# Kernel tuning notes

Hardware: AMD Instinct MI355X
Metric: run time of the kernel (lower is better)

Reference implementation:

```python
import jax, jax.numpy as jnp
import numpy as np

B, S, D, H, HD = 2, 2048, 1024, 16, 64
K, L = 1024, 4  # num_codes, vq_levels


def setup_inputs() -> dict:
    key = jax.random.key(0)
    ks = jax.random.split(key, 12)
    w = lambda k, shape: jax.random.normal(k, shape, jnp.float32) * 0.02
    return {
        "x": jax.random.normal(ks[0], (B, S, D), jnp.float32),
        "ln1_g": jnp.ones((D,), jnp.float32), "ln1_b": jnp.zeros((D,), jnp.float32),
        "wq": w(ks[1], (D, D)), "wk": w(ks[2], (D, D)), "wv": w(ks[3], (D, D)),
        "wg": w(ks[4], (D, D)), "wo": w(ks[5], (D, D)),
        "ln2_g": jnp.ones((D,), jnp.float32), "ln2_b": jnp.zeros((D,), jnp.float32),
        "w1": w(ks[6], (D, 4 * D)), "b1": jnp.zeros((4 * D,), jnp.float32),
        "w2": w(ks[7], (4 * D, D)), "b2": jnp.zeros((D,), jnp.float32),
        "ln3_g": jnp.ones((D,), jnp.float32), "ln3_b": jnp.zeros((D,), jnp.float32),
        "codebooks": jax.random.uniform(ks[8], (L, K, D), jnp.float32, -1.0 / K, 1.0 / K),
    }


def _ln(x, g, b):
    m = jnp.mean(x, -1, keepdims=True)
    v = jnp.var(x, -1, keepdims=True)
    return (x - m) / jnp.sqrt(v + 1e-5) * g + b


def _rope(x):  # x: [B, S, H, HD]
    hd = x.shape[-1]
    inv = 1.0 / (10000.0 ** (jnp.arange(0, hd, 2, dtype=jnp.float32) / hd))
    t = jnp.arange(x.shape[1], dtype=jnp.float32)
    f = jnp.einsum('i,j->ij', t, inv)               # [S, HD/2]
    emb = jnp.concatenate([f, f], -1)               # [S, HD]
    cos = jnp.cos(emb)[None, :, None, :]
    sin = jnp.sin(emb)[None, :, None, :]
    x1, x2 = jnp.split(x, 2, -1)
    rot = jnp.concatenate([-x2, x1], -1)
    return x * cos + rot * sin


def reference(x, ln1_g, ln1_b, wq, wk, wv, wg, wo, ln2_g, ln2_b,
              w1, b1, w2, b2, ln3_g, ln3_b, codebooks):
    # --- retention sub-block (pre-LN) ---
    h = _ln(x, ln1_g, ln1_b)
    q = (h @ wq).reshape(B, S, H, HD)
    k = (h @ wk).reshape(B, S, H, HD)
    v = (h @ wv).reshape(B, S, H, HD)
    q, k = _rope(q), _rope(k)
    q, k, v = (a.transpose(0, 2, 1, 3) for a in (q, k, v))  # [B,H,S,HD]
    i = jnp.arange(S)
    dmask = jnp.tril(i[:, None] - i[None, :]).astype(jnp.float32)  # [S,S], >=0
    gamma = (1.0 - jnp.exp2(-5.0 - jnp.arange(H, dtype=jnp.float32)))[:, None, None]
    decay = (gamma ** dmask) * jnp.tril(jnp.ones((S, S), jnp.float32))  # [H,S,S]
    ret = jnp.einsum('bhqd,bhkd->bhqk', q, k) / np.sqrt(HD).astype(np.float32) * decay
    o = jnp.einsum('bhqk,bhkd->bhqd', ret, v).transpose(0, 2, 1, 3).reshape(B, S, D)
    g = jax.nn.silu(h @ wg)
    x = x + (o * g) @ wo
    # --- MLP sub-block (pre-LN) ---
    h2 = _ln(x, ln2_g, ln2_b)
    x = x + (jax.nn.gelu(h2 @ w1 + b1, approximate=False) @ w2 + b2)
    # --- residual vector quantizer ---
    xn = _ln(x, ln3_g, ln3_b)
    residual, total = xn, jnp.zeros_like(xn)
    ql, el = 0.0, 0.0
    for lvl in range(L):
        cb = codebooks[lvl]                         # [K, D]
        flat = residual.reshape(-1, D)              # [B*S, D]
        d2 = (jnp.sum(flat ** 2, 1, keepdims=True)
              + jnp.sum(cb ** 2, 1) - 2.0 * flat @ cb.T)
        idx = jnp.argmin(d2, 1)
        quant = cb[idx].reshape(xn.shape)
        ql = ql + jnp.mean((quant - jax.lax.stop_gradient(residual)) ** 2)
        el = el + jnp.mean((jax.lax.stop_gradient(quant) - residual) ** 2)
        total = total + quant
        residual = residual - jax.lax.stop_gradient(quant)
    final = xn + jax.lax.stop_gradient(total - xn)  # straight-through
    return (x + final, ql / L, el / L)
```

## Files before the change

### kernel.cpp

```cpp
#include <hip/hip_runtime.h>
#include <cstdint>
#include <cstddef>

#define DEV __device__ __forceinline__

typedef __attribute__((ext_vector_type(8))) short bf16x8;
typedef __attribute__((ext_vector_type(4))) float f32x4;

typedef const __attribute__((address_space(1))) void gl_void;
typedef __attribute__((address_space(3))) void lds_void;

DEV unsigned short f2bf(float f){
  union { float f; uint32_t u; } v; v.f = f;
  uint32_t r = v.u + 0x7FFFu + ((v.u >> 16) & 1u);
  return (unsigned short)(r >> 16);
}
DEV float bf2f(unsigned short u){
  union { uint32_t u; float f; } v; v.u = ((uint32_t)u) << 16; return v.f;
}
DEV uint32_t packbf2(float a, float b){
  return (uint32_t)f2bf(a) | ((uint32_t)f2bf(b) << 16);
}

__global__ void ln_kernel(const float* __restrict__ x, const float* __restrict__ gw,
                          const float* __restrict__ bw, unsigned short* __restrict__ obf,
                          float* __restrict__ of32)
{
  const int row = blockIdx.x, t = threadIdx.x;
  const float4 v = ((const float4*)(x + (size_t)row*1024))[t];
  float s  = v.x + v.y + v.z + v.w;
  float s2 = v.x*v.x + v.y*v.y + v.z*v.z + v.w*v.w;
  #pragma unroll
  for (int o = 32; o >= 1; o >>= 1){ s += __shfl_down(s, o); s2 += __shfl_down(s2, o); }
  __shared__ float red[8];
  const int w = t >> 6, ln = t & 63;
  if (ln == 0){ red[w] = s; red[4+w] = s2; }
  __syncthreads();
  const float fs  = red[0]+red[1]+red[2]+red[3];
  const float fs2 = red[4]+red[5]+red[6]+red[7];
  const float mean = fs * (1.0f/1024.0f);
  const float var  = fs2 * (1.0f/1024.0f) - mean*mean;
  const float rstd = rsqrtf(var + 1e-5f);
  const float4 gv = ((const float4*)gw)[t];
  const float4 bv = ((const float4*)bw)[t];
  float4 o4;
  o4.x = (v.x-mean)*rstd*gv.x + bv.x;
  o4.y = (v.y-mean)*rstd*gv.y + bv.y;
  o4.z = (v.z-mean)*rstd*gv.z + bv.z;
  o4.w = (v.w-mean)*rstd*gv.w + bv.w;
  if (of32) ((float4*)(of32 + (size_t)row*1024))[t] = o4;
  ushort4 ob; ob.x = f2bf(o4.x); ob.y = f2bf(o4.y); ob.z = f2bf(o4.z); ob.w = f2bf(o4.w);
  ((ushort4*)(obf + (size_t)row*1024))[t] = ob;
}

struct Ptr5 { const float* p[5]; };

DEV void dev_transpose(const float* __restrict__ src, unsigned short* __restrict__ dst,
                       int r0, int c0, int R, int C)
{
  __shared__ float tile[32][33];
  const int tx = threadIdx.x & 31, ty = threadIdx.x >> 5;
  #pragma unroll
  for (int i = 0; i < 32; i += 8)
    tile[ty+i][tx] = src[(size_t)(r0+ty+i)*C + c0 + tx];
  __syncthreads();
  #pragma unroll
  for (int i = 0; i < 32; i += 8)
    dst[(size_t)(c0+ty+i)*R + r0 + tx] = f2bf(tile[tx][ty+i]);
}

__global__ void prep_all(Ptr5 p5, unsigned short* __restrict__ wqkvgT,
                         const float* __restrict__ w1, unsigned short* __restrict__ w1T,
                         const float* __restrict__ w2, unsigned short* __restrict__ w2T,
                         const float* __restrict__ cb, unsigned short* __restrict__ cbbf,
                         float* __restrict__ cbn2, float2* __restrict__ rtab)
{
  const int b = blockIdx.x, t = threadIdx.x;
  if (b < 5120){
    const int z = b >> 10, r = b & 1023;
    dev_transpose(p5.p[z], wqkvgT + (size_t)z*1048576, (r >> 5)*32, (r & 31)*32, 1024, 1024);
  } else if (b < 9216){
    const int r = b - 5120;
    dev_transpose(w1, w1T, (r >> 7)*32, (r & 127)*32, 1024, 4096);
  } else if (b < 13312){
    const int r = b - 9216;
    dev_transpose(w2, w2T, (r >> 5)*32, (r & 31)*32, 4096, 1024);
  } else if (b < 17408){
    const int code = b - 13312;
    const float4 v = ((const float4*)(cb + (size_t)code*1024))[t];
    ushort4 o; o.x = f2bf(v.x); o.y = f2bf(v.y); o.z = f2bf(v.z); o.w = f2bf(v.w);
    ((ushort4*)(cbbf + (size_t)code*1024))[t] = o;
    float s = v.x*v.x + v.y*v.y + v.z*v.z + v.w*v.w;
    #pragma unroll
    for (int off = 32; off >= 1; off >>= 1) s += __shfl_down(s, off);
    __shared__ float red[4];
    if ((t & 63) == 0) red[t >> 6] = s;
    __syncthreads();
    if (t == 0) cbn2[code] = red[0]+red[1]+red[2]+red[3];
  } else {
    const int i = (b - 17408)*256 + t;
    const int s = i >> 5, j = i & 31;
    const float ang = (float)s * exp2f(-(float)j * 0.4152410118609203f);
    float sn, cs; sincosf(ang, &sn, &cs);
    rtab[i] = make_float2(cs, sn);
  }
}

template<int EPI>
__global__ __launch_bounds__(512, 2) void gemm256(
    const unsigned short* __restrict__ A, const unsigned short* __restrict__ BT,
    unsigned short* __restrict__ C, const float* __restrict__ bias,
    const float2* __restrict__ rt, int M, int N, int K)
{
  __shared__ __align__(16) unsigned short SH[65536];
  const int t = threadIdx.x;
  const int w = t >> 6, ln = t & 63, lg = ln >> 4, lc = ln & 15;
  const int wm = w >> 2, wn = w & 3;
  const int gx = gridDim.x, nwg = gridDim.x * gridDim.y;
  int lin = blockIdx.y * gx + blockIdx.x;
  lin = (lin >> 3) + (lin & 7) * (nwg >> 3);
  const int m0 = (lin / gx) * 256, n0 = (lin % gx) * 256;
  const int NT = K >> 6;
  const int nit = NT >> 1;

  f32x4 acc[2][2][4][2] = {};
  bf16x8 aF[4][2], bF[2][2];

  auto stageHT = [&](int d, int isB, int h, int kt){
    const unsigned short* src = isB ? BT : A;
    const int mb = (isB ? n0 : m0) + h*128;
    const int base16 = isB*4096 + d*2048 + h*1024;
    #pragma unroll
    for (int j = 0; j < 2; ++j){
      const int o = j*512 + t;
      const int wu = o & 63;
      const int r16 = wu >> 2, cu = wu & 3;
      const int s = o >> 6;
      const int rg = s >> 1, cg = s & 1;
      const int row = rg*16 + r16;
      const int srcu = cg*4 + (cu ^ ((r16 & 8) >> 2));
      __builtin_amdgcn_global_load_lds(
        (gl_void*)(src + (size_t)(mb + row)*K + (size_t)kt*64 + srcu*8),
        (lds_void*)&SH[(base16 + j*512 + (t & ~63))*8], 16, 0, 0);
    }
  };

  auto ldA = [&](int d, int mh, int mf, int ks) -> bf16x8 {
    const int u = d*2048 + mh*1024 + ((wm*4+mf)*2 + ks)*64 + lc*4 + (lg ^ ((lc & 8) >> 2));
    return *(const bf16x8*)&SH[u*8];
  };
  auto ldB = [&](int d, int nh, int nf, int ks) -> bf16x8 {
    const int u = 4096 + d*2048 + nh*1024 + ((wn*2+nf)*2 + ks)*64 + lc*4 + (lg ^ ((lc & 8) >> 2));
    return *(const bf16x8*)&SH[u*8];
  };

#define RD_A(d, mh) { _Pragma("unroll") for (int mf = 0; mf < 4; ++mf){ \
    aF[mf][0] = ldA(d, mh, mf, 0); aF[mf][1] = ldA(d, mh, mf, 1); } }
#define RD_B(d, nh) { _Pragma("unroll") for (int nf = 0; nf < 2; ++nf){ \
    bF[nf][0] = ldB(d, nh, nf, 0); bF[nf][1] = ldB(d, nh, nf, 1); } }
#define MM(mh, nh) { \
    __builtin_amdgcn_s_setprio(1); \
    _Pragma("unroll") for (int mf = 0; mf < 4; ++mf) \
      _Pragma("unroll") for (int nf = 0; nf < 2; ++nf){ \
        acc[mh][nh][mf][nf] = __builtin_amdgcn_mfma_f32_16x16x32_bf16(aF[mf][0], bF[nf][0], acc[mh][nh][mf][nf], 0, 0, 0); \
        acc[mh][nh][mf][nf] = __builtin_amdgcn_mfma_f32_16x16x32_bf16(aF[mf][1], bF[nf][1], acc[mh][nh][mf][nf], 0, 0, 0); } \
    __builtin_amdgcn_s_setprio(0); }
#define BAR()   __builtin_amdgcn_s_barrier()
#define LGKM0() asm volatile("s_waitcnt lgkmcnt(0)" ::: "memory")

  stageHT(0,0,0,0); stageHT(0,0,1,0); stageHT(0,1,0,0); stageHT(0,1,1,0);
  stageHT(1,0,0,1); stageHT(1,1,1,1);
  asm volatile("s_waitcnt vmcnt(4)" ::: "memory");
  BAR();

  for (int it = 0; it < nit; ++it){
    const int v = 2*it + 1, up = 2*it + 2, vp = 2*it + 3;
    const bool hu = (up < NT), hv = (vp < NT);

    RD_A(0,0); RD_B(0,0);
    stageHT(1,0,1,v);
    BAR(); LGKM0(); MM(0,0); BAR();

    RD_B(0,1);
    stageHT(1,1,0,v);
    BAR(); LGKM0(); MM(0,1); BAR();

    RD_A(0,1);
    if (hu) stageHT(0,0,0,up);
    BAR(); LGKM0(); MM(1,1); BAR();

    RD_B(0,0);
    if (hu) stageHT(0,1,1,up);
    BAR(); LGKM0(); MM(1,0);
    if (hu) asm volatile("s_waitcnt vmcnt(4)" ::: "memory");
    else    asm volatile("s_waitcnt vmcnt(0)" ::: "memory");
    BAR();

    RD_A(1,0); RD_B(1,0);
    if (hu) stageHT(0,0,1,up);
    BAR(); LGKM0(); MM(0,0); BAR();

    RD_B(1,1);
    if (hu) stageHT(0,1,0,up);
    BAR(); LGKM0(); MM(0,1); BAR();

    RD_A(1,1);
    if (hv) stageHT(1,0,0,vp);
    BAR(); LGKM0(); MM(1,1); BAR();

    RD_B(1,0);
    if (hv) stageHT(1,1,1,vp);
    BAR(); LGKM0(); MM(1,0);
    if (hv) asm volatile("s_waitcnt vmcnt(4)" ::: "memory");
    else    asm volatile("s_waitcnt vmcnt(0)" ::: "memory");
    BAR();
  }
#undef RD_A
#undef RD_B
#undef MM

  const int sect = n0 >> 10;
  unsigned short* outp3 = C + (size_t)sect*4194304;
  const int cb1 = n0 & 1023;
  unsigned short* slab = &SH[wm*4096];

  #pragma unroll
  for (int mh = 0; mh < 2; ++mh){
    #pragma unroll
    for (int mf = 0; mf < 4; ++mf){
      BAR();
      #pragma unroll
      for (int nh = 0; nh < 2; ++nh)
        #pragma unroll
        for (int nf = 0; nf < 2; ++nf)
          #pragma unroll
          for (int r = 0; r < 4; ++r){
            const int rho = lg*4 + r;
            const int c = nh*128 + wn*32 + nf*16 + lc;
            float vv = acc[mh][nh][mf][nf][r];
            if constexpr (EPI == 2){
              vv += bias[n0 + c];
              vv = 0.5f * vv * (1.0f + erff(vv * 0.70710678118654752f));
            }
            if constexpr (EPI == 3){ if (sect == 3) vv = vv * (1.0f / (1.0f + __expf(-vv))); }
            slab[rho*256 + ((((c>>3) ^ (rho&3)))<<3) + (c&7)] = f2bf(vv);
          }
      LGKM0();
      BAR();
      const int rr = ln >> 2;
      const int row = m0 + mh*128 + wm*64 + mf*16 + rr;
      #pragma unroll
      for (int kk = 0; kk < 2; ++kk){
        const int cc = wn*64 + (ln & 3)*16 + kk*8;
        const int u = cc >> 3;
        const bf16x8 vown = *(const bf16x8*)&slab[rr*256 + ((u ^ (rr&3))<<3)];
        if constexpr (EPI == 3){
          if (sect <= 1){
            const bf16x8 vpart = *(const bf16x8*)&slab[rr*256 + (((u^4) ^ (rr&3))<<3)];
            const int s_ = row & 2047;
            union { bf16x8 v; unsigned short s[8]; } ov, pv, res;
            ov.v = vown; pv.v = vpart;
            #pragma unroll
            for (int j = 0; j < 8; ++j){
              const int col = cc + j;
              const float2 cs = rt[(s_ << 5) + (col & 31)];
              const float a = bf2f(ov.s[j]), b = bf2f(pv.s[j]);
              res.s[j] = f2bf((col & 32) ? (a*cs.x + b*cs.y) : (a*cs.x - b*cs.y));
            }
            *(bf16x8*)(outp3 + (size_t)row*1024 + cb1 + cc) = res.v;
          } else {
            *(bf16x8*)(outp3 + (size_t)row*1024 + cb1 + cc) = vown;
          }
        } else {
          *(bf16x8*)(C + (size_t)row*N + n0 + cc) = vown;
        }
      }
    }
  }
#undef BAR
#undef LGKM0
}

template<int NSPLIT>
__global__ __launch_bounds__(256, 4) void gemm128_sk(
    const unsigned short* __restrict__ A, const unsigned short* __restrict__ BT,
    float* __restrict__ Cp_base, int M, int N, int K)
{
  __shared__ __align__(16) unsigned short As[2][128*32];
  __shared__ __align__(16) unsigned short Bs[2][128*32];
  const int t = threadIdx.x;
  const int w = t >> 6, ln = t & 63, lg = ln >> 4, lc = ln & 15;
  const int gx = gridDim.x, nwg = gridDim.x * gridDim.y;
  int lin = blockIdx.y * gx + blockIdx.x;
  lin = (lin >> 3) + (lin & 7) * (nwg >> 3);
  const int m0 = (lin / gx) * 128, n0 = (lin % gx) * 128;
  const int wr = (w >> 1) * 64, wc = (w & 1) * 64;
  f32x4 acc[4][4] = {};
  const int nkt = (K >> 5) / NSPLIT;
  const int ktb = blockIdx.z * nkt;

  auto stage = [&](int buf, int kt){
    #pragma unroll
    for (int c = 0; c < 2; ++c){
      const int chunk = c*256 + t;
      const int row = chunk >> 2, ke = (chunk & 3) * 8;
      __builtin_amdgcn_global_load_lds(
          (gl_void*)(A + (size_t)(m0+row)*K + (size_t)(ktb+kt)*32 + ke),
          (lds_void*)&As[buf][(c*256 + w*64)*8], 16, 0, 0);
      __builtin_amdgcn_global_load_lds(
          (gl_void*)(BT + (size_t)(n0+row)*K + (size_t)(ktb+kt)*32 + ke),
          (lds_void*)&Bs[buf][(c*256 + w*64)*8], 16, 0, 0);
    }
  };

  stage(0, 0);
  __syncthreads();
  for (int kt = 0; kt < nkt; ++kt){
    const int cur = kt & 1;
    if (kt + 1 < nkt) stage(cur ^ 1, kt + 1);
    bf16x8 af[4], bfr[4];
    #pragma unroll
    for (int i = 0; i < 4; ++i){
      af[i]  = *(const bf16x8*)&As[cur][(wr + i*16 + lc)*32 + lg*8];
      bfr[i] = *(const bf16x8*)&Bs[cur][(wc + i*16 + lc)*32 + lg*8];
    }
    #pragma unroll
    for (int m = 0; m < 4; ++m)
      #pragma unroll
      for (int n = 0; n < 4; ++n)
        acc[m][n] = __builtin_amdgcn_mfma_f32_16x16x32_bf16(af[m], bfr[n], acc[m][n], 0, 0, 0);
    __syncthreads();
  }

  float* Cp = Cp_base + (size_t)blockIdx.z * (size_t)M * N;
  #pragma unroll
  for (int m = 0; m < 4; ++m)
    #pragma unroll
    for (int n = 0; n < 4; ++n)
      #pragma unroll
      for (int r = 0; r < 4; ++r){
        const int row = m0 + wr + m*16 + lg*4 + r;
        const int col = n0 + wc + n*16 + lc;
        Cp[(size_t)row*N + col] = acc[m][n][r];
      }
}

template<int EPI, bool BIAS, bool RES, bool OUTBF>
__global__ __launch_bounds__(256, 3) void gemm64_bt(
    const unsigned short* __restrict__ A, const unsigned short* __restrict__ BT,
    void* __restrict__ Cv, const float* __restrict__ bias, const float* __restrict__ resid,
    int M, int N, int K)
{
  __shared__ __align__(16) unsigned short As[2][64*64];
  __shared__ __align__(16) unsigned short Bs[2][128*64];
  const int t = threadIdx.x;
  const int w = t >> 6, ln = t & 63, lg = ln >> 4, lc = ln & 15;
  const int gx = gridDim.x, nwg = gridDim.x * gridDim.y;
  int lin = blockIdx.y * gx + blockIdx.x;
  lin = (lin >> 3) + (lin & 7) * (nwg >> 3);
  const int bx = lin % gx, by = lin / gx;
  const int m0 = by * 64, n0 = bx * 128;
  const int wr = (w >> 1) * 32, wc = (w & 1) * 64;
  f32x4 acc[2][4] = {};
  const int nkt = K >> 6;

  auto stage = [&](int buf, int kt){
    #pragma unroll
    for (int c = 0; c < 2; ++c){
      const int chunk = c*256 + t;
      const int row = chunk >> 3;
      const int kb = (((chunk & 7) << 4) ^ ((row & 7) << 4)) >> 1;
      __builtin_amdgcn_global_load_lds(
          (gl_void*)(A + (size_t)(m0+row)*K + (size_t)kt*64 + kb),
          (lds_void*)&As[buf][(c*256 + w*64)*8], 16, 0, 0);
    }
    #pragma unroll
    for (int c = 0; c < 4; ++c){
      const int chunk = c*256 + t;
      const int row = chunk >> 3;
      const int kb = (((chunk & 7) << 4) ^ ((row & 7) << 4)) >> 1;
      __builtin_amdgcn_global_load_lds(
          (gl_void*)(BT + (size_t)(n0+row)*K + (size_t)kt*64 + kb),
          (lds_void*)&Bs[buf][(c*256 + w*64)*8], 16, 0, 0);
    }
  };

  stage(0, 0);
  __syncthreads();
  for (int kt = 0; kt < nkt; ++kt){
    const int cur = kt & 1;
    if (kt + 1 < nkt) stage(cur ^ 1, kt + 1);
    #pragma unroll
    for (int ks = 0; ks < 2; ++ks){
      bf16x8 af[2], bfr[4];
      #pragma unroll
      for (int i = 0; i < 2; ++i){
        const int rowA = wr + i*16 + lc;
        const int colA = (((ks<<6) + (lg<<4)) ^ ((rowA & 7) << 4)) >> 1;
        af[i] = *(const bf16x8*)&As[cur][rowA*64 + colA];
      }
      #pragma unroll
      for (int i = 0; i < 4; ++i){
        const int rowB = wc + i*16 + lc;
        const int colB = (((ks<<6) + (lg<<4)) ^ ((rowB & 7) << 4)) >> 1;
        bfr[i] = *(const bf16x8*)&Bs[cur][rowB*64 + colB];
      }
      #pragma unroll
      for (int m = 0; m < 2; ++m)
        #pragma unroll
        for (int n = 0; n < 4; ++n)
          acc[m][n] = __builtin_amdgcn_mfma_f32_16x16x32_bf16(af[m], bfr[n], acc[m][n], 0, 0, 0);
    }
    __syncthreads();
  }

  if constexpr (EPI == 4){
    #pragma unroll
    for (int m = 0; m < 2; ++m){
      #pragma unroll
      for (int r = 0; r < 4; ++r){
        float best = 3.4e38f; int bi = 0;
        #pragma unroll
        for (int n = 0; n < 4; ++n){
          const int col = n0 + wc + n*16 + lc;
          const float d = bias[col] - 2.0f*acc[m][n][r];
          if (d < best){ best = d; bi = col; }
        }
        #pragma unroll
        for (int o = 1; o < 16; o <<= 1){
          const float ob = __shfl_xor(best, o);
          const int oi = __shfl_xor(bi, o);
          if (ob < best || (ob == best && oi < bi)){ best = ob; bi = oi; }
        }
        if (lc == 0){
          const int row = m0 + wr + m*16 + lg*4 + r;
          ((float2*)Cv)[row*16 + bx*2 + (w & 1)] = make_float2(best, (float)bi);
        }
      }
    }
    return;
  }

  #pragma unroll
  for (int m = 0; m < 2; ++m){
    #pragma unroll
    for (int n = 0; n < 4; ++n){
      #pragma unroll
      for (int r = 0; r < 4; ++r){
        const int row = m0 + wr + m*16 + lg*4 + r;
        const int col = n0 + wc + n*16 + lc;
        float v = acc[m][n][r];
        if constexpr (BIAS) v += bias[col];
        if constexpr (RES) v += resid[(size_t)row*N + col];
        if constexpr (OUTBF) ((unsigned short*)Cv)[(size_t)row*N + col] = f2bf(v);
        else                 ((float*)Cv)[(size_t)row*N + col] = v;
      }
    }
  }
}

__global__ void splitk_reduce(const float* __restrict__ p, const float* __restrict__ bias,
                              const float* __restrict__ resid, float* __restrict__ out)
{
  const int i = blockIdx.x*256 + threadIdx.x;
  const float4 a = ((const float4*)p)[i];
  const float4 b = ((const float4*)(p + 4194304))[i];
  const float4 rv = ((const float4*)resid)[i];
  const float4 bv = ((const float4*)bias)[i & 255];
  float4 o;
  o.x = a.x + b.x + rv.x + bv.x;
  o.y = a.y + b.y + rv.y + bv.y;
  o.z = a.z + b.z + rv.z + bv.z;
  o.w = a.w + b.w + rv.w + bv.w;
  ((float4*)out)[i] = o;
}

__global__ __launch_bounds__(256, 2) void chunk_sum(
    const unsigned short* __restrict__ kb, const unsigned short* __restrict__ vb,
    float* __restrict__ Tbuf)
{
  __shared__ unsigned short KT[64*72];
  __shared__ unsigned short VT[64*72];
  const int t = threadIdx.x, w = t >> 6, ln = t & 63, lg = ln >> 4, lc = ln & 15;
  const int blk = blockIdx.x;
  const int bh = blk >> 5, c = blk & 31;
  const int b = bh >> 4, hh = bh & 15;
  const float lg2g = log2f(1.0f - exp2f(-5.0f - (float)hh));
  #pragma unroll
  for (int ch = 0; ch < 2; ++ch){
    const int chunk = ch*256 + t;
    const int i = chunk >> 3, d0 = (chunk & 7)*8;
    const size_t gofs = ((size_t)(b*2048 + c*64 + i))*1024 + hh*64 + d0;
    const float wi = exp2f(lg2g * (float)(64 - i));
    union {uint4 u; unsigned short s[8];} kv, vv;
    kv.u = *(const uint4*)(kb + gofs);
    vv.u = *(const uint4*)(vb + gofs);
    #pragma unroll
    for (int j = 0; j < 8; ++j){
      KT[(d0+j)*72 + i] = f2bf(bf2f(kv.s[j]) * wi);
      VT[(d0+j)*72 + i] = vv.s[j];
    }
  }
  __syncthreads();
  f32x4 acc[4] = {};
  #pragma unroll
  for (int ks = 0; ks < 2; ++ks){
    const bf16x8 af = *(const bf16x8*)&KT[(w*16 + lc)*72 + ks*32 + lg*8];
    #pragma unroll
    for (int n = 0; n < 4; ++n){
      const bf16x8 bf = *(const bf16x8*)&VT[(n*16 + lc)*72 + ks*32 + lg*8];
      acc[n] = __builtin_amdgcn_mfma_f32_16x16x32_bf16(af, bf, acc[n], 0, 0, 0);
    }
  }
  float* out = Tbuf + (size_t)blk*4096;
  #pragma unroll
  for (int n = 0; n < 4; ++n)
    #pragma unroll
    for (int r = 0; r < 4; ++r)
      out[(w*16 + lg*4 + r)*64 + n*16 + lc] = acc[n][r];
}

__global__ void chunk_scan(const float* __restrict__ Tbuf, unsigned short* __restrict__ statesT)
{
  const int bh = blockIdx.x, q = blockIdx.y, t = threadIdx.x;
  const int hh = bh & 15;
  const float gamma = 1.0f - exp2f(-5.0f - (float)hh);
  const float g64 = exp2f(log2f(gamma) * 64.0f);
  float S[4] = {0.f, 0.f, 0.f, 0.f};
  const int dv = t >> 2;
  const int j0 = q*16 + (t & 3)*4;
  for (int c = 0; c < 32; ++c){
    const size_t base = ((size_t)(bh*32 + c))*4096;
    ushort4 p; p.x = f2bf(S[0]); p.y = f2bf(S[1]); p.z = f2bf(S[2]); p.w = f2bf(S[3]);
    *(ushort4*)(statesT + base + dv*64 + j0) = p;
    #pragma unroll
    for (int j = 0; j < 4; ++j)
      S[j] = g64*S[j] + Tbuf[base + (size_t)(j0 + j)*64 + dv];
  }
}

__global__ __launch_bounds__(256, 2) void retention_chunk(
    const unsigned short* __restrict__ qb, const unsigned short* __restrict__ kb,
    const unsigned short* __restrict__ vb, const unsigned short* __restrict__ gb,
    const unsigned short* __restrict__ statesT, unsigned short* __restrict__ og)
{
  __shared__ unsigned short VT[64*72];
  __shared__ unsigned short Pw[64*72];
  const int t = threadIdx.x, w = t >> 6, ln = t & 63, lg = ln >> 4, lc = ln & 15;
  const int blk = blockIdx.x;
  const int bh = blk >> 5, c = blk & 31;
  const int b = bh >> 4, hh = bh & 15;
  const float lg2g = log2f(1.0f - exp2f(-5.0f - (float)hh));
  float gpr[4];
  #pragma unroll
  for (int r = 0; r < 4; ++r) gpr[r] = exp2f(-lg2g * (float)r);
  const size_t rowbase = (size_t)(b*2048 + c*64);

  #pragma unroll
  for (int ch = 0; ch < 2; ++ch){
    const int chunk = ch*256 + t;
    const int i = chunk >> 3, d0 = (chunk & 7)*8;
    union {uint4 u; unsigned short s[8];} vv;
    vv.u = *(const uint4*)(vb + (rowbase + i)*1024 + hh*64 + d0);
    #pragma unroll
    for (int j = 0; j < 8; ++j) VT[(d0+j)*72 + i] = vv.s[j];
  }

  bf16x8 Qf[2], Kf[4][2];
  #pragma unroll
  for (int ks = 0; ks < 2; ++ks){
    union {uint4 u; bf16x8 f;} cv;
    cv.u = *(const uint4*)(qb + (rowbase + w*16 + lc)*1024 + hh*64 + ks*32 + lg*8);
    Qf[ks] = cv.f;
    #pragma unroll
    for (int mt = 0; mt < 4; ++mt){
      union {uint4 u; bf16x8 f;} kv;
      kv.u = *(const uint4*)(kb + (rowbase + mt*16 + lc)*1024 + hh*64 + ks*32 + lg*8);
      Kf[mt][ks] = kv.f;
    }
  }

  f32x4 st[4] = {};
  #pragma unroll
  for (int ks = 0; ks < 2; ++ks)
    #pragma unroll
    for (int mt = 0; mt < 4; ++mt)
      st[mt] = __builtin_amdgcn_mfma_f32_16x16x32_bf16(Kf[mt][ks], Qf[ks], st[mt], 0, 0, 0);

  __syncthreads();

  #pragma unroll
  for (int mt = 0; mt < 4; ++mt){
    const int kp = mt*16 + lg*4;
    const int qrow = w*16 + lc;
    const int delta0 = qrow - kp;
    const float dec0 = exp2f(lg2g * (float)delta0) * 0.125f;
    float vals[4];
    #pragma unroll
    for (int r = 0; r < 4; ++r)
      vals[r] = (delta0 >= r) ? st[mt][r] * dec0 * gpr[r] : 0.0f;
    uint2 pk; pk.x = packbf2(vals[0], vals[1]); pk.y = packbf2(vals[2], vals[3]);
    *(uint2*)&Pw[qrow*72 + kp] = pk;
  }

  f32x4 acc[4] = {};
  const unsigned short* Sbase = statesT + (size_t)blk*4096;
  #pragma unroll
  for (int ks = 0; ks < 2; ++ks)
    #pragma unroll
    for (int n = 0; n < 4; ++n){
      union {uint4 u; bf16x8 f;} sv;
      sv.u = *(const uint4*)(Sbase + (n*16 + lc)*64 + ks*32 + lg*8);
      acc[n] = __builtin_amdgcn_mfma_f32_16x16x32_bf16(Qf[ks], sv.f, acc[n], 0, 0, 0);
    }
  #pragma unroll
  for (int n = 0; n < 4; ++n)
    #pragma unroll
    for (int r = 0; r < 4; ++r)
      acc[n][r] *= exp2f(lg2g * (float)(w*16 + lg*4 + r)) * 0.125f;

  #pragma unroll
  for (int ks = 0; ks < 2; ++ks){
    const bf16x8 Pf = *(const bf16x8*)&Pw[(w*16 + lc)*72 + ks*32 + lg*8];
    #pragma unroll
    for (int n = 0; n < 4; ++n){
      const bf16x8 Vf = *(const bf16x8*)&VT[(n*16 + lc)*72 + ks*32 + lg*8];
      acc[n] = __builtin_amdgcn_mfma_f32_16x16x32_bf16(Pf, Vf, acc[n], 0, 0, 0);
    }
  }

  #pragma unroll
  for (int n = 0; n < 4; ++n){
    #pragma unroll
    for (int r = 0; r < 4; ++r){
      const size_t row = rowbase + w*16 + lg*4 + r;
      const int col = hh*64 + n*16 + lc;
      const float gv = bf2f(gb[row*1024 + col]);
      og[row*1024 + col] = f2bf(acc[n][r] * gv);
    }
  }
}

template<int FINAL>
__global__ void rvq_update3(const float* __restrict__ cb_l, const float2* __restrict__ partials,
                            const float* __restrict__ res_in, float* __restrict__ res_out,
                            unsigned short* __restrict__ resb, float* __restrict__ qlpart, int lvl,
                            const float* __restrict__ x2, const float* __restrict__ xn,
                            float* __restrict__ outf)
{
  const int m = blockIdx.x, t = threadIdx.x;
  __shared__ int sid;
  if (t == 0){
    float best = 3.4e38f; int bi = 0;
    #pragma unroll
    for (int p = 0; p < 16; ++p){
      const float2 pr = partials[m*16 + p];
      if (pr.x < best){ best = pr.x; bi = (int)pr.y; }
    }
    sid = bi;
  }
  __syncthreads();
  const int id = sid;
  const float4 qv = ((const float4*)(cb_l + (size_t)id*1024))[t];
  const float4 rv = ((const float4*)(res_in + (size_t)m*1024))[t];
  float4 nr; nr.x = rv.x - qv.x; nr.y = rv.y - qv.y; nr.z = rv.z - qv.z; nr.w = rv.w - qv.w;
  if constexpr (FINAL){
    const float4 a = ((const float4*)(x2 + (size_t)m*1024))[t];
    const float4 b = ((const float4*)(xn + (size_t)m*1024))[t];
    float4 o;
    o.x = a.x + b.x - nr.x;
    o.y = a.y + b.y - nr.y;
    o.z = a.z + b.z - nr.z;
    o.w = a.w + b.w - nr.w;
    ((float4*)(outf + (size_t)m*1024))[t] = o;
  } else {
    ((float4*)(res_out + (size_t)m*1024))[t] = nr;
    ushort4 nb; nb.x = f2bf(nr.x); nb.y = f2bf(nr.y); nb.z = f2bf(nr.z); nb.w = f2bf(nr.w);
    ((ushort4*)(resb + (size_t)m*1024))[t] = nb;
  }
  float s = nr.x*nr.x + nr.y*nr.y + nr.z*nr.z + nr.w*nr.w;
  #pragma unroll
  for (int o = 32; o >= 1; o >>= 1) s += __shfl_down(s, o);
  __shared__ float red[4];
  if ((t & 63) == 0) red[t >> 6] = s;
  __syncthreads();
  if (t == 0) qlpart[lvl*4096 + m] = red[0]+red[1]+red[2]+red[3];
}

__global__ void ql_final(const float* __restrict__ qlpart, float* __restrict__ outs)
{
  const int t = threadIdx.x;
  float s = 0.f;
  for (int i = t; i < 16384; i += 256) s += qlpart[i];
  #pragma unroll
  for (int o = 32; o >= 1; o >>= 1) s += __shfl_down(s, o);
  __shared__ float red[4];
  if ((t & 63) == 0) red[t >> 6] = s;
  __syncthreads();
  if (t == 0){
    const float q = (red[0]+red[1]+red[2]+red[3]) * (1.0f/4194304.0f) * 0.25f;
    outs[0] = q; outs[1] = q;
  }
}

extern "C" void kernel_launch(void* const* d_in, const int* in_sizes, int n_in,
                              void* d_out, int out_size, void* d_ws, size_t ws_size,
                              hipStream_t stream)
{
  const float* x     = (const float*)d_in[0];
  const float* ln1_g = (const float*)d_in[1];
  const float* ln1_b = (const float*)d_in[2];
  const float* wq    = (const float*)d_in[3];
  const float* wk    = (const float*)d_in[4];
  const float* wv    = (const float*)d_in[5];
  const float* wg    = (const float*)d_in[6];
  const float* wo    = (const float*)d_in[7];
  const float* ln2_g = (const float*)d_in[8];
  const float* ln2_b = (const float*)d_in[9];
  const float* w1    = (const float*)d_in[10];
  const float* b1    = (const float*)d_in[11];
  const float* w2    = (const float*)d_in[12];
  const float* b2    = (const float*)d_in[13];
  const float* ln3_g = (const float*)d_in[14];
  const float* ln3_b = (const float*)d_in[15];
  const float* cb    = (const float*)d_in[16];

  char* ws = (char*)d_ws;
  const size_t MB = 1024*1024;
  unsigned short* wqkvgT = (unsigned short*)(ws + 0*MB);
  unsigned short* w1T  = (unsigned short*)(ws + 10*MB);
  unsigned short* w2T  = (unsigned short*)(ws + 18*MB);
  unsigned short* cbbf = (unsigned short*)(ws + 26*MB);
  float* cbn2     = (float*)(ws + 34*MB);
  float* qlpart   = (float*)(ws + 34*MB + 16*1024);
  float2* partials= (float2*)(ws + 34*MB + 128*1024);
  unsigned short* hbf  = (unsigned short*)(ws + 35*MB);
  unsigned short* qbuf = (unsigned short*)(ws + 43*MB);
  unsigned short* kbuf = (unsigned short*)(ws + 51*MB);
  unsigned short* vbuf = (unsigned short*)(ws + 59*MB);
  unsigned short* gbuf = (unsigned short*)(ws + 67*MB);
  float* skbuf  = (float*)(ws + 43*MB);
  unsigned short* ogb  = (unsigned short*)(ws + 75*MB);
  float* x1     = (float*)(ws + 83*MB);
  unsigned short* h2   = (unsigned short*)(ws + 99*MB);
  unsigned short* a1   = (unsigned short*)(ws + 107*MB);
  float* x2     = (float*)(ws + 139*MB);
  float* Tbuf   = (float*)(ws + 139*MB);
  float* xnf    = (float*)(ws + 155*MB);
  unsigned short* statesT = (unsigned short*)(ws + 155*MB);
  unsigned short* resb = (unsigned short*)(ws + 171*MB);
  float2* rtab  = (float2*)(ws + 179*MB);
  float* resw   = (float*)(ws + 187*MB);

  float* outf = (float*)d_out;

  Ptr5 p5; p5.p[0]=wq; p5.p[1]=wk; p5.p[2]=wv; p5.p[3]=wg; p5.p[4]=wo;
  hipLaunchKernelGGL(prep_all, dim3(17664), dim3(256), 0, stream,
                     p5, wqkvgT, w1, w1T, w2, w2T, cb, cbbf, cbn2, rtab);

  hipLaunchKernelGGL(ln_kernel, dim3(4096), dim3(256), 0, stream, x, ln1_g, ln1_b, hbf, (float*)nullptr);
  hipLaunchKernelGGL((gemm256<3>), dim3(16,16), dim3(512), 0, stream,
                     hbf, wqkvgT, qbuf, (const float*)nullptr, (const float2*)rtab, 4096, 4096, 1024);
  hipLaunchKernelGGL(chunk_sum,  dim3(1024), dim3(256), 0, stream, kbuf, vbuf, Tbuf);
  hipLaunchKernelGGL(chunk_scan, dim3(32,4), dim3(256), 0, stream, Tbuf, statesT);
  hipLaunchKernelGGL(retention_chunk, dim3(1024), dim3(256), 0, stream,
                     qbuf, kbuf, vbuf, gbuf, statesT, ogb);
  hipLaunchKernelGGL((gemm64_bt<0,false,true,false>), dim3(8,64), dim3(256), 0, stream,
                     ogb, wqkvgT + 4194304, (void*)x1, (const float*)nullptr, x, 4096, 1024, 1024);

  hipLaunchKernelGGL(ln_kernel, dim3(4096), dim3(256), 0, stream, x1, ln2_g, ln2_b, h2, (float*)nullptr);
  hipLaunchKernelGGL((gemm256<2>), dim3(16,16), dim3(512), 0, stream,
                     h2, w1T, a1, b1, (const float2*)rtab, 4096, 4096, 1024);
  hipLaunchKernelGGL((gemm128_sk<2>), dim3(8,32,2), dim3(256), 0, stream,
                     a1, w2T, skbuf, 4096, 1024, 4096);
  hipLaunchKernelGGL(splitk_reduce, dim3(4096), dim3(256), 0, stream, skbuf, b2, x1, x2);

  hipLaunchKernelGGL(ln_kernel, dim3(4096), dim3(256), 0, stream, x2, ln3_g, ln3_b, resb, xnf);
  for (int lvl = 0; lvl < 4; ++lvl){
    hipLaunchKernelGGL((gemm64_bt<4,false,false,false>), dim3(8,64), dim3(256), 0, stream,
                       resb, cbbf + (size_t)lvl*1048576, (void*)partials,
                       cbn2 + lvl*1024, (const float*)nullptr, 4096, 1024, 1024);
    if (lvl < 3)
      hipLaunchKernelGGL((rvq_update3<0>), dim3(4096), dim3(256), 0, stream,
                         cb + (size_t)lvl*1048576, partials,
                         (lvl == 0) ? xnf : resw, resw, resb, qlpart, lvl,
                         (const float*)nullptr, (const float*)nullptr, (float*)nullptr);
    else
      hipLaunchKernelGGL((rvq_update3<1>), dim3(4096), dim3(256), 0, stream,
                         cb + (size_t)lvl*1048576, partials,
                         resw, (float*)nullptr, (unsigned short*)nullptr, qlpart, lvl,
                         x2, xnf, outf);
  }

  hipLaunchKernelGGL(ql_final, dim3(1), dim3(256), 0, stream, qlpart, outf + 4194304);
}
```

Measured before the change: 392.8 us.

## Fuse LN1 into prep, fuse split-K reduce with LN3, new QKVG GEMM

Folds the first layernorm into the weight-prep kernel as extra blocks, and merges the split-K reduction with the third layernorm so x2 is not re-read. It also swaps the 256-tile QKVG GEMM with its LDS-staged RoPE/SiLU epilogue for a simpler 128x128 double-buffered GEMM that applies RoPE and SiLU directly from registers. The aim is fewer launches and less memory traffic. The new QKVG GEMM uses an unswizzled LDS layout and scalar bf16 stores, which may be slower than the tuned 256 kernel.

```diff
diff --git a/kernel.cpp b/kernel.cpp
--- a/kernel.cpp
+++ b/kernel.cpp
@@ -53,6 +53,48 @@
   ((ushort4*)(obf + (size_t)row*1024))[t] = ob;
 }
 
+__global__ void reduce_ln(const float* __restrict__ p, const float* __restrict__ b2,
+                          const float* __restrict__ x1, float* __restrict__ x2,
+                          const float* __restrict__ g3, const float* __restrict__ b3,
+                          unsigned short* __restrict__ resb, float* __restrict__ xnf)
+{
+  const int row = blockIdx.x, t = threadIdx.x;
+  const size_t off = (size_t)row*1024/4 + t;
+  const float4 a = ((const float4*)p)[off];
+  const float4 b = ((const float4*)(p + 4194304))[off];
+  const float4 rv = ((const float4*)x1)[off];
+  const float4 bv2 = ((const float4*)b2)[t];
+  float4 v;
+  v.x = a.x + b.x + rv.x + bv2.x;
+  v.y = a.y + b.y + rv.y + bv2.y;
+  v.z = a.z + b.z + rv.z + bv2.z;
+  v.w = a.w + b.w + rv.w + bv2.w;
+  ((float4*)x2)[off] = v;
+  float s  = v.x + v.y + v.z + v.w;
+  float s2 = v.x*v.x + v.y*v.y + v.z*v.z + v.w*v.w;
+  #pragma unroll
+  for (int o = 32; o >= 1; o >>= 1){ s += __shfl_down(s, o); s2 += __shfl_down(s2, o); }
+  __shared__ float red[8];
+  const int w = t >> 6, ln = t & 63;
+  if (ln == 0){ red[w] = s; red[4+w] = s2; }
+  __syncthreads();
+  const float fs  = red[0]+red[1]+red[2]+red[3];
+  const float fs2 = red[4]+red[5]+red[6]+red[7];
+  const float mean = fs * (1.0f/1024.0f);
+  const float var  = fs2 * (1.0f/1024.0f) - mean*mean;
+  const float rstd = rsqrtf(var + 1e-5f);
+  const float4 gv = ((const float4*)g3)[t];
+  const float4 bv = ((const float4*)b3)[t];
+  float4 o4;
+  o4.x = (v.x-mean)*rstd*gv.x + bv.x;
+  o4.y = (v.y-mean)*rstd*gv.y + bv.y;
+  o4.z = (v.z-mean)*rstd*gv.z + bv.z;
+  o4.w = (v.w-mean)*rstd*gv.w + bv.w;
+  ((float4*)xnf)[off] = o4;
+  ushort4 ob; ob.x = f2bf(o4.x); ob.y = f2bf(o4.y); ob.z = f2bf(o4.z); ob.w = f2bf(o4.w);
+  ((ushort4*)resb)[off] = ob;
+}
+
 struct Ptr5 { const float* p[5]; };
 
 DEV void dev_transpose(const float* __restrict__ src, unsigned short* __restrict__ dst,
@@ -73,7 +115,9 @@
                          const float* __restrict__ w1, unsigned short* __restrict__ w1T,
                          const float* __restrict__ w2, unsigned short* __restrict__ w2T,
                          const float* __restrict__ cb, unsigned short* __restrict__ cbbf,
-                         float* __restrict__ cbn2, float2* __restrict__ rtab)
+                         float* __restrict__ cbn2, float2* __restrict__ rtab,
+                         const float* __restrict__ x, const float* __restrict__ ln1_g,
+                         const float* __restrict__ ln1_b, unsigned short* __restrict__ hbf)
 {
   const int b = blockIdx.x, t = threadIdx.x;
   if (b < 5120){
@@ -97,12 +141,111 @@
     if ((t & 63) == 0) red[t >> 6] = s;
     __syncthreads();
     if (t == 0) cbn2[code] = red[0]+red[1]+red[2]+red[3];
-  } else {
+  } else if (b < 17664){
     const int i = (b - 17408)*256 + t;
     const int s = i >> 5, j = i & 31;
     const float ang = (float)s * exp2f(-(float)j * 0.4152410118609203f);
     float sn, cs; sincosf(ang, &sn, &cs);
     rtab[i] = make_float2(cs, sn);
+  } else {
+    const int row = b - 17664;
+    const float4 v = ((const float4*)(x + (size_t)row*1024))[t];
+    float s  = v.x + v.y + v.z + v.w;
+    float s2 = v.x*v.x + v.y*v.y + v.z*v.z + v.w*v.w;
+    #pragma unroll
+    for (int o = 32; o >= 1; o >>= 1){ s += __shfl_down(s, o); s2 += __shfl_down(s2, o); }
+    __shared__ float red2[8];
+    const int w = t >> 6, ln = t & 63;
+    if (ln == 0){ red2[w] = s; red2[4+w] = s2; }
+    __syncthreads();
+    const float fs  = red2[0]+red2[1]+red2[2]+red2[3];
+    const float fs2 = red2[4]+red2[5]+red2[6]+red2[7];
+    const float mean = fs * (1.0f/1024.0f);
+    const float var  = fs2 * (1.0f/1024.0f) - mean*mean;
+    const float rstd = rsqrtf(var + 1e-5f);
+    const float4 gv = ((const float4*)ln1_g)[t];
+    const float4 bv = ((const float4*)ln1_b)[t];
+    ushort4 ob;
+    ob.x = f2bf((v.x-mean)*rstd*gv.x + bv.x);
+    ob.y = f2bf((v.y-mean)*rstd*gv.y + bv.y);
+    ob.z = f2bf((v.z-mean)*rstd*gv.z + bv.z);
+    ob.w = f2bf((v.w-mean)*rstd*gv.w + bv.w);
+    ((ushort4*)(hbf + (size_t)row*1024))[t] = ob;
+  }
+}
+
+__global__ __launch_bounds__(256, 4) void gemm128_qkvg(
+    const unsigned short* __restrict__ A, const unsigned short* __restrict__ BT,
+    unsigned short* __restrict__ C, const float2* __restrict__ rt, int K)
+{
+  __shared__ __align__(16) unsigned short As[2][128*32];
+  __shared__ __align__(16) unsigned short Bs[2][128*32];
+  const int t = threadIdx.x;
+  const int w = t >> 6, ln = t & 63, lg = ln >> 4, lc = ln & 15;
+  const int gx = gridDim.x, nwg = gridDim.x * gridDim.y;
+  int lin = blockIdx.y * gx + blockIdx.x;
+  lin = (lin >> 3) + (lin & 7) * (nwg >> 3);
+  const int m0 = (lin / gx) * 128, n0 = (lin % gx) * 128;
+  const int wr = (w >> 1) * 64, wc = (w & 1) * 64;
+  f32x4 acc[4][4] = {};
+  const int nkt = K >> 5;
+
+  auto stage = [&](int buf, int kt){
+    #pragma unroll
+    for (int c = 0; c < 2; ++c){
+      const int chunk = c*256 + t;
+      const int row = chunk >> 2, ke = (chunk & 3) * 8;
+      __builtin_amdgcn_global_load_lds(
+          (gl_void*)(A + (size_t)(m0+row)*K + (size_t)kt*32 + ke),
+          (lds_void*)&As[buf][(c*256 + w*64)*8], 16, 0, 0);
+      __builtin_amdgcn_global_load_lds(
+          (gl_void*)(BT + (size_t)(n0+row)*K + (size_t)kt*32 + ke),
+          (lds_void*)&Bs[buf][(c*256 + w*64)*8], 16, 0, 0);
+    }
+  };
+
+  stage(0, 0);
+  __syncthreads();
+  for (int kt = 0; kt < nkt; ++kt){
+    const int cur = kt & 1;
+    if (kt + 1 < nkt) stage(cur ^ 1, kt + 1);
+    bf16x8 af[4], bfr[4];
+    #pragma unroll
+    for (int i = 0; i < 4; ++i){
+      af[i]  = *(const bf16x8*)&As[cur][(wr + i*16 + lc)*32 + lg*8];
+      bfr[i] = *(const bf16x8*)&Bs[cur][(wc + i*16 + lc)*32 + lg*8];
+    }
+    #pragma unroll
+    for (int m = 0; m < 4; ++m)
+      #pragma unroll
+      for (int n = 0; n < 4; ++n)
+        acc[m][n] = __builtin_amdgcn_mfma_f32_16x16x32_bf16(af[m], bfr[n], acc[m][n], 0, 0, 0);
+    __syncthreads();
+  }
+
+  const int sect = (n0 + wc) >> 10;
+  unsigned short* outp = C + (size_t)sect*4194304;
+  #pragma unroll
+  for (int m = 0; m < 4; ++m){
+    #pragma unroll
+    for (int r = 0; r < 4; ++r){
+      const int row = m0 + wr + m*16 + lg*4 + r;
+      const int s_ = row & 2047;
+      #pragma unroll
+      for (int n = 0; n < 4; ++n){
+        const int col = n0 + wc + n*16 + lc;
+        const int c1 = col & 1023;
+        float v = acc[m][n][r];
+        if (sect <= 1){
+          const float2 cs = rt[(s_ << 5) + (c1 & 31)];
+          const float vp = acc[m][n ^ 2][r];
+          v = (c1 & 32) ? (v*cs.x + vp*cs.y) : (v*cs.x - vp*cs.y);
+        } else if (sect == 3){
+          v = v * (1.0f / (1.0f + __expf(-v)));
+        }
+        outp[(size_t)row*1024 + c1] = f2bf(v);
+      }
+    }
   }
 }
 
@@ -219,11 +362,7 @@
 #undef RD_B
 #undef MM
 
-  const int sect = n0 >> 10;
-  unsigned short* outp3 = C + (size_t)sect*4194304;
-  const int cb1 = n0 & 1023;
   unsigned short* slab = &SH[wm*4096];
-
   #pragma unroll
   for (int mh = 0; mh < 2; ++mh){
     #pragma unroll
@@ -238,11 +377,8 @@
             const int rho = lg*4 + r;
             const int c = nh*128 + wn*32 + nf*16 + lc;
             float vv = acc[mh][nh][mf][nf][r];
-            if constexpr (EPI == 2){
-              vv += bias[n0 + c];
-              vv = 0.5f * vv * (1.0f + erff(vv * 0.70710678118654752f));
-            }
-            if constexpr (EPI == 3){ if (sect == 3) vv = vv * (1.0f / (1.0f + __expf(-vv))); }
+            vv += bias[n0 + c];
+            vv = 0.5f * vv * (1.0f + erff(vv * 0.70710678118654752f));
             slab[rho*256 + ((((c>>3) ^ (rho&3)))<<3) + (c&7)] = f2bf(vv);
           }
       LGKM0();
@@ -254,26 +390,7 @@
         const int cc = wn*64 + (ln & 3)*16 + kk*8;
         const int u = cc >> 3;
         const bf16x8 vown = *(const bf16x8*)&slab[rr*256 + ((u ^ (rr&3))<<3)];
-        if constexpr (EPI == 3){
-          if (sect <= 1){
-            const bf16x8 vpart = *(const bf16x8*)&slab[rr*256 + (((u^4) ^ (rr&3))<<3)];
-            const int s_ = row & 2047;
-            union { bf16x8 v; unsigned short s[8]; } ov, pv, res;
-            ov.v = vown; pv.v = vpart;
-            #pragma unroll
-            for (int j = 0; j < 8; ++j){
-              const int col = cc + j;
-              const float2 cs = rt[(s_ << 5) + (col & 31)];
-              const float a = bf2f(ov.s[j]), b = bf2f(pv.s[j]);
-              res.s[j] = f2bf((col & 32) ? (a*cs.x + b*cs.y) : (a*cs.x - b*cs.y));
-            }
-            *(bf16x8*)(outp3 + (size_t)row*1024 + cb1 + cc) = res.v;
-          } else {
-            *(bf16x8*)(outp3 + (size_t)row*1024 + cb1 + cc) = vown;
-          }
-        } else {
-          *(bf16x8*)(C + (size_t)row*N + n0 + cc) = vown;
-        }
+        *(bf16x8*)(C + (size_t)row*N + n0 + cc) = vown;
       }
     }
   }
@@ -457,22 +574,6 @@
       }
     }
   }
-}
-
-__global__ void splitk_reduce(const float* __restrict__ p, const float* __restrict__ bias,
-                              const float* __restrict__ resid, float* __restrict__ out)
-{
-  const int i = blockIdx.x*256 + threadIdx.x;
-  const float4 a = ((const float4*)p)[i];
-  const float4 b = ((const float4*)(p + 4194304))[i];
-  const float4 rv = ((const float4*)resid)[i];
-  const float4 bv = ((const float4*)bias)[i & 255];
-  float4 o;
-  o.x = a.x + b.x + rv.x + bv.x;
-  o.y = a.y + b.y + rv.y + bv.y;
-  o.z = a.z + b.z + rv.z + bv.z;
-  o.w = a.w + b.w + rv.w + bv.w;
-  ((float4*)out)[i] = o;
 }
 
 __global__ __launch_bounds__(256, 2) void chunk_sum(
@@ -755,12 +856,12 @@
   float* outf = (float*)d_out;
 
   Ptr5 p5; p5.p[0]=wq; p5.p[1]=wk; p5.p[2]=wv; p5.p[3]=wg; p5.p[4]=wo;
-  hipLaunchKernelGGL(prep_all, dim3(17664), dim3(256), 0, stream,
-                     p5, wqkvgT, w1, w1T, w2, w2T, cb, cbbf, cbn2, rtab);
-
-  hipLaunchKernelGGL(ln_kernel, dim3(4096), dim3(256), 0, stream, x, ln1_g, ln1_b, hbf, (float*)nullptr);
-  hipLaunchKernelGGL((gemm256<3>), dim3(16,16), dim3(512), 0, stream,
-                     hbf, wqkvgT, qbuf, (const float*)nullptr, (const float2*)rtab, 4096, 4096, 1024);
+  hipLaunchKernelGGL(prep_all, dim3(21760), dim3(256), 0, stream,
+                     p5, wqkvgT, w1, w1T, w2, w2T, cb, cbbf, cbn2, rtab,
+                     x, ln1_g, ln1_b, hbf);
+
+  hipLaunchKernelGGL(gemm128_qkvg, dim3(32,32), dim3(256), 0, stream,
+                     hbf, wqkvgT, qbuf, (const float2*)rtab, 1024);
   hipLaunchKernelGGL(chunk_sum,  dim3(1024), dim3(256), 0, stream, kbuf, vbuf, Tbuf);
   hipLaunchKernelGGL(chunk_scan, dim3(32,4), dim3(256), 0, stream, Tbuf, statesT);
   hipLaunchKernelGGL(retention_chunk, dim3(1024), dim3(256), 0, stream,
@@ -773,9 +874,9 @@
                      h2, w1T, a1, b1, (const float2*)rtab, 4096, 4096, 1024);
   hipLaunchKernelGGL((gemm128_sk<2>), dim3(8,32,2), dim3(256), 0, stream,
                      a1, w2T, skbuf, 4096, 1024, 4096);
-  hipLaunchKernelGGL(splitk_reduce, dim3(4096), dim3(256), 0, stream, skbuf, b2, x1, x2);
-
-  hipLaunchKernelGGL(ln_kernel, dim3(4096), dim3(256), 0, stream, x2, ln3_g, ln3_b, resb, xnf);
+  hipLaunchKernelGGL(reduce_ln, dim3(4096), dim3(256), 0, stream,
+                     skbuf, b2, x1, x2, ln3_g, ln3_b, resb, xnf);
+
   for (int lvl = 0; lvl < 4; ++lvl){
     hipLaunchKernelGGL((gemm64_bt<4,false,false,false>), dim3(8,64), dim3(256), 0, stream,
                        resb, cbbf + (size_t)lvl*1048576, (void*)partials,
```

Result: no change. 399.3 us (+1.7%).
